# Optimization experiments

Measured on AMD Instinct MI355X. Metric: run time of the kernel, lower is better.

The kernel has to match this reference:

```python
import jax, jax.numpy as jnp
import numpy as np

D_MODEL = 1024
N_HEADS = 16
HEAD_DIM = D_MODEL // N_HEADS


def setup_inputs() -> dict:
    key = jax.random.key(0)
    k_x, k_qkv, k_out = jax.random.split(key, 3)
    B, T = 4, 2048
    x = jax.random.normal(k_x, (B, T, D_MODEL), dtype=jnp.float32)
    # nn.Linear weight is (out, in); we store transposed (in, out) for x @ W
    s = 1.0 / np.sqrt(D_MODEL)
    W_qkv = jax.random.uniform(k_qkv, (D_MODEL, 3 * D_MODEL), dtype=jnp.float32, minval=-s, maxval=s)
    W_out = jax.random.uniform(k_out, (D_MODEL, D_MODEL), dtype=jnp.float32, minval=-s, maxval=s)
    return {"x": x, "W_qkv": W_qkv, "W_out": W_out}


def reference(x, W_qkv, W_out):
    B, T, C = x.shape
    H, Dh = N_HEADS, HEAD_DIM
    qkv = x @ W_qkv                                   # (B,T,3C)
    q, k, v = jnp.split(qkv, 3, axis=-1)
    # (B,T,C) -> (B,H,T,Dh)
    def split_heads(t):
        return t.reshape(B, T, H, Dh).transpose(0, 2, 1, 3)
    q, k, v = split_heads(q), split_heads(k), split_heads(v)
    scale = 1.0 / np.sqrt(Dh).astype(np.float32)
    scores = jnp.einsum('bhqd,bhkd->bhqk', q, k) * scale  # (B,H,T,T)
    causal = jnp.triu(jnp.ones((T, T), dtype=bool), k=1)   # True above diag
    scores = jnp.where(causal, -jnp.inf, scores)
    attn = jax.nn.softmax(scores, axis=-1)
    out = jnp.einsum('bhqk,bhkd->bhqd', attn, v)       # (B,H,T,Dh)
    out = out.transpose(0, 2, 1, 3).reshape(B, T, C)
    return out @ W_out
```

## Files before the change

kernel.cpp:

```cpp
#include <hip/hip_runtime.h>
#include <stdint.h>

#define T_ 2048
#define BB_ 4

typedef __bf16 bf16x8 __attribute__((ext_vector_type(8)));
typedef float f32x4 __attribute__((ext_vector_type(4)));
typedef unsigned short u16x8 __attribute__((ext_vector_type(8)));
typedef unsigned int u32x2 __attribute__((ext_vector_type(2)));
typedef unsigned int u32x4 __attribute__((ext_vector_type(4)));

__device__ __forceinline__ unsigned short f2b(float f) {
    unsigned int u = __builtin_bit_cast(unsigned int, f);
    return (unsigned short)((u + 0x7fffu + ((u >> 16) & 1u)) >> 16);
}

__device__ __forceinline__ unsigned cvt_pk(float lo, float hi) {
    unsigned r;
    asm("v_cvt_pk_bf16_f32 %0, %1, %2" : "=v"(r) : "v"(lo), "v"(hi));
    return r;
}

__device__ __forceinline__ void gload16(const void* g, const void* lds) {
    __builtin_amdgcn_global_load_lds(
        (__attribute__((address_space(1))) void*)(uintptr_t)g,
        (__attribute__((address_space(3))) void*)(uintptr_t)(unsigned int)(uintptr_t)lds,
        16, 0, 0);
}

__device__ __forceinline__ bf16x8 ld_b8(const unsigned short* p) {
    return *(const bf16x8*)p;
}

#define MFMA16(a, b, c) __builtin_amdgcn_mfma_f32_16x16x32_bf16((a), (b), (c), 0, 0, 0)

__global__ __launch_bounds__(256) void k_cvt(const float* __restrict__ in,
                                             unsigned short* __restrict__ out, int n) {
    int i = (blockIdx.x * 256 + threadIdx.x) * 4;
    const int stride = gridDim.x * 256 * 4;
    for (; i < n; i += stride) {
        const float4 v = *(const float4*)(in + i);
        ushort4 o = make_ushort4(f2b(v.x), f2b(v.y), f2b(v.z), f2b(v.w));
        *(ushort4*)(out + i) = o;
    }
}

template <int K, int N>
__global__ __launch_bounds__(256) void k_cvt_T(const float* __restrict__ W,
                                               unsigned short* __restrict__ WT) {
    __shared__ unsigned short t_[64][72];
    const int nt = blockIdx.x % (N / 64), kt = blockIdx.x / (N / 64);
    const int tid = threadIdx.x;
    const int r = tid >> 2, c = (tid & 3) * 16;
    const float* src = W + (size_t)(kt * 64 + r) * N + nt * 64 + c;
#pragma unroll
    for (int j = 0; j < 16; j += 4) {
        float4 v = *(const float4*)(src + j);
        t_[r][c + j + 0] = f2b(v.x);
        t_[r][c + j + 1] = f2b(v.y);
        t_[r][c + j + 2] = f2b(v.z);
        t_[r][c + j + 3] = f2b(v.w);
    }
    __syncthreads();
    unsigned short* dst = WT + (size_t)(nt * 64 + r) * K + kt * 64 + c;
#pragma unroll
    for (int j = 0; j < 16; ++j) dst[j] = t_[c + j][r];
}

template <int MODE, int NCOLS>
__global__ __launch_bounds__(512, 2) void k_gemm256(
    const unsigned short* __restrict__ A, const unsigned short* __restrict__ Bt,
    void* __restrict__ Cv, unsigned short* __restrict__ vt2) {
    constexpr int K = 1024, NT = K / 64;
    __shared__ unsigned short Abuf[3][2][8192];
    __shared__ unsigned short Bbuf[3][8192];
    const int tid = threadIdx.x;
    const int lane = tid & 63, wid = tid >> 6;
    const int wr = wid >> 1, wc = wid & 1;
    const int l4 = lane >> 4, l15 = lane & 15;
    const int bid = blockIdx.y * gridDim.x + blockIdx.x;
    const int cpx = (gridDim.x * gridDim.y) >> 3;
    const int nb = (bid & 7) * cpx + (bid >> 3);
    const int m0 = (nb / gridDim.x) * 256, n0 = (nb % gridDim.x) * 128;

    const int se0 = tid * 8, se1 = tid * 8 + 4096;
    const int r0_ = se0 >> 6, c0_ = (se0 & 63) ^ ((r0_ & 7) << 3);
    const int r1_ = se1 >> 6, c1_ = (se1 & 63) ^ ((r1_ & 7) << 3);

    f32x4 acc[4][4] = {};

    auto STAGE1 = [&](int t, int d) {
        const unsigned short* as = A + (size_t)m0 * K + t * 64;
        gload16(as + (size_t)r0_ * K + c0_, &Abuf[d][0][se0]);
        gload16(as + (size_t)r1_ * K + c1_, &Abuf[d][0][se1]);
        const unsigned short* bs = Bt + (size_t)n0 * K + t * 64;
        gload16(bs + (size_t)r0_ * K + c0_, &Bbuf[d][se0]);
    };
    auto STAGE2 = [&](int t, int d) {
        const unsigned short* as = A + (size_t)(m0 + 128) * K + t * 64;
        gload16(as + (size_t)r0_ * K + c0_, &Abuf[d][1][se0]);
        gload16(as + (size_t)r1_ * K + c1_, &Abuf[d][1][se1]);
        const unsigned short* bs = Bt + (size_t)n0 * K + t * 64;
        gload16(bs + (size_t)r1_ * K + c1_, &Bbuf[d][se1]);
    };

    auto swz = [](const unsigned short* base, int row, int col) {
        int byte = row * 128 + col * 2;
        byte ^= (row & 7) << 4;
        return (const unsigned short*)((const char*)base + byte);
    };

    STAGE1(0, 0);
    STAGE2(0, 0);
    STAGE1(1, 1);
    STAGE2(1, 1);
    int d = 0;
    for (int t = 0; t < NT; ++t) {
        if (t == NT - 1)
            asm volatile("s_waitcnt vmcnt(0)" ::: "memory");
        else
            asm volatile("s_waitcnt vmcnt(6)" ::: "memory");
        __builtin_amdgcn_sched_barrier(0);
        __builtin_amdgcn_s_barrier();
        __builtin_amdgcn_sched_barrier(0);
        const int dn = (d + 2 >= 3) ? d - 1 : d + 2;
        if (t + 2 < NT) STAGE1(t + 2, dn);
        __builtin_amdgcn_sched_barrier(0);
        const unsigned short* Ah = &Abuf[d][wr >> 1][0];
        const unsigned short* Bh = &Bbuf[d][0];
        bf16x8 af[2][4], bfr[2][4];
#pragma unroll
        for (int ks = 0; ks < 2; ++ks) {
#pragma unroll
            for (int m = 0; m < 4; ++m)
                af[ks][m] =
                    ld_b8(swz(Ah, (wr & 1) * 64 + m * 16 + l15, ks * 32 + l4 * 8));
#pragma unroll
            for (int n = 0; n < 4; ++n)
                bfr[ks][n] = ld_b8(swz(Bh, wc * 64 + n * 16 + l15, ks * 32 + l4 * 8));
        }
        __builtin_amdgcn_s_setprio(1);
#pragma unroll
        for (int m = 0; m < 4; ++m)
#pragma unroll
            for (int n = 0; n < 4; ++n)
                acc[m][n] = MFMA16(af[0][m], bfr[0][n], acc[m][n]);
        __builtin_amdgcn_s_setprio(0);
        __builtin_amdgcn_sched_barrier(0);
        if (t + 2 < NT) STAGE2(t + 2, dn);
        __builtin_amdgcn_sched_barrier(0);
        __builtin_amdgcn_s_setprio(1);
#pragma unroll
        for (int m = 0; m < 4; ++m)
#pragma unroll
            for (int n = 0; n < 4; ++n)
                acc[m][n] = MFMA16(af[1][m], bfr[1][n], acc[m][n]);
        __builtin_amdgcn_s_setprio(0);
        d = (d + 1 == 3) ? 0 : d + 1;
    }

    const int crow0 = m0 + wr * 64 + l4 * 4;
    const int ccol0 = n0 + wc * 64 + l15;
    if (MODE == 0 && n0 >= 2048) {
#pragma unroll
        for (int m = 0; m < 4; ++m)
#pragma unroll
            for (int n = 0; n < 4; ++n) {
                const int row = crow0 + m * 16;
                const int c = ccol0 + n * 16 - 2048;
                const int b = row >> 11, tt = row & 2047;
                const int h = c >> 6, dh = c & 63;
                ushort4 o;
                o.x = f2b(acc[m][n][0]);
                o.y = f2b(acc[m][n][1]);
                o.z = f2b(acc[m][n][2]);
                o.w = f2b(acc[m][n][3]);
                *(ushort4*)(vt2 + (size_t)(b * 16 + h) * 131072 + (tt >> 2) * 256 +
                            dh * 4) = o;
            }
    } else {
#pragma unroll
        for (int m = 0; m < 4; ++m)
#pragma unroll
            for (int n = 0; n < 4; ++n)
#pragma unroll
                for (int r = 0; r < 4; ++r) {
                    const size_t idx =
                        (size_t)(crow0 + m * 16 + r) * NCOLS + ccol0 + n * 16;
                    if (MODE == 1)
                        ((float*)Cv)[idx] = acc[m][n][r];
                    else
                        ((unsigned short*)Cv)[idx] = f2b(acc[m][n][r]);
                }
    }
}

__global__ __launch_bounds__(512) void k_attn(const unsigned short* __restrict__ qkv,
                                              const unsigned short* __restrict__ vt2,
                                              unsigned short* __restrict__ ao) {
    __shared__ unsigned short Ks[2 * 4096];
    __shared__ unsigned short Vs[2 * 4096];
    const int bh = blockIdx.x & 63;
    const int p = blockIdx.x >> 6;
    const int b = bh >> 4, h = bh & 15;
    const int tid = threadIdx.x, lane = tid & 63, w = tid >> 6;
    const int l4 = lane >> 4, l15 = lane & 15;
    const int wrow = w * 16 + l15;

    const int sr0 = w * 8 + (lane >> 3);
    const int scol = 8 * ((lane & 7) ^ (lane >> 3));
    const unsigned short* Kg = qkv + (size_t)(b * T_) * 3072 + 1024 + h * 64;

    const unsigned short* Vg = vt2 + (size_t)bh * 131072;
    const int sv = w * 2 + (lane >> 5);
    const unsigned short* vsrcw =
        Vg + (4 * (sv & 3) + (sv >> 2)) * 256 + (lane & 31) * 8;

    const u32x4 onesw = {0x3f803f80u, 0x3f803f80u, 0x3f803f80u, 0x3f803f80u};
    const bf16x8 ones = __builtin_bit_cast(bf16x8, onesw);

    for (int half = 0; half < 2; ++half) {
        const int qq = half ? p : 15 - p;

        const unsigned short* qb =
            qkv + (size_t)(b * T_ + qq * 128 + wrow) * 3072 + h * 64;
        bf16x8 qf0, qf1;
        {
            const bf16x8 r0 = ld_b8(qb + l4 * 8);
            const bf16x8 r1 = ld_b8(qb + 32 + l4 * 8);
#pragma unroll
            for (int j = 0; j < 8; ++j) {
                qf0[j] = (__bf16)((float)r0[j] * 0.18033688f);
                qf1[j] = (__bf16)((float)r1[j] * 0.18033688f);
            }
        }

        f32x4 o[4] = {};
        f32x4 o_l = {};

        auto STAGE = [&](int kt, int bi) {
            gload16(Kg + (size_t)(kt * 64 + sr0) * 3072 + scol,
                    Ks + bi * 4096 + w * 512);
            gload16(vsrcw + (size_t)kt * 4096, Vs + bi * 4096 + w * 512);
        };

        auto COMPUTE = [&](int bi, int dk) {
            const unsigned short* Kb = Ks + bi * 4096;
            const unsigned short* Vb = Vs + bi * 4096;
            float tv[4][4];
            __builtin_amdgcn_s_setprio(1);
#pragma unroll
            for (int i = 0; i < 4; ++i) {
                const int key = i * 16 + l15;
                const int sw = (key & 7) << 4;
                const bf16x8 kf0 = ld_b8(Kb + (key * 128 + ((l4 * 16) ^ sw)) / 2);
                const bf16x8 kf1 = ld_b8(Kb + (key * 128 + ((l4 * 16 + 64) ^ sw)) / 2);
                f32x4 sacc = {};
                sacc = MFMA16(kf0, qf0, sacc);
                sacc = MFMA16(kf1, qf1, sacc);
#pragma unroll
                for (int r = 0; r < 4; ++r) tv[i][r] = sacc[r];
            }
            __builtin_amdgcn_s_setprio(0);
            if (dk >= 0) {
                const int base = dk * 64 - wrow;
#pragma unroll
                for (int i = 0; i < 4; ++i)
#pragma unroll
                    for (int r = 0; r < 4; ++r)
                        if (base + i * 16 + l4 * 4 + r > 0) tv[i][r] = -1e30f;
            }
            unsigned pw[8];
#pragma unroll
            for (int i = 0; i < 4; ++i) {
                float pv[4];
#pragma unroll
                for (int r = 0; r < 4; ++r) pv[r] = __builtin_amdgcn_exp2f(tv[i][r]);
                pw[i * 2 + 0] = cvt_pk(pv[0], pv[1]);
                pw[i * 2 + 1] = cvt_pk(pv[2], pv[3]);
            }
            __builtin_amdgcn_s_setprio(1);
#pragma unroll
            for (int st = 0; st < 2; ++st) {
                const u32x4 pk = {pw[st * 4 + 0], pw[st * 4 + 1], pw[st * 4 + 2],
                                  pw[st * 4 + 3]};
                const bf16x8 pf = __builtin_bit_cast(bf16x8, pk);
                o_l = MFMA16(pf, ones, o_l);
#pragma unroll
                for (int ni = 0; ni < 4; ++ni) {
                    const unsigned short* vb =
                        Vb + (l4 * 4 + st * 2) * 256 + (ni * 16 + l15) * 4;
                    const u32x2 va = *(const u32x2*)vb;
                    const u32x2 vc = *(const u32x2*)(vb + 256);
                    const u32x4 vv = {va.x, va.y, vc.x, vc.y};
                    const bf16x8 vf = __builtin_bit_cast(bf16x8, vv);
                    o[ni] = MFMA16(pf, vf, o[ni]);
                }
            }
            __builtin_amdgcn_s_setprio(0);
        };

        const int NTI = 2 * qq + 1;
        __syncthreads();
        STAGE(0, 0);
        __syncthreads();
        for (int kt = 0; kt < NTI; ++kt) {
            STAGE(kt + 1, (kt + 1) & 1);
            COMPUTE(kt & 1, kt - 2 * qq);
            __syncthreads();
        }
        COMPUTE(NTI & 1, 1);

        unsigned short* aop =
            ao + (size_t)(b * T_ + qq * 128 + w * 16) * 1024 + h * 64;
#pragma unroll
        for (int r = 0; r < 4; ++r) {
            const float inv = 1.0f / o_l[r];
#pragma unroll
            for (int ni = 0; ni < 4; ++ni)
                aop[(size_t)(l4 * 4 + r) * 1024 + ni * 16 + l15] = f2b(o[ni][r] * inv);
        }
    }
}

extern "C" void kernel_launch(void* const* d_in, const int* in_sizes, int n_in,
                              void* d_out, int out_size, void* d_ws, size_t ws_size,
                              hipStream_t stream) {
    (void)in_sizes; (void)n_in; (void)out_size; (void)ws_size;
    const float* x = (const float*)d_in[0];
    const float* Wqkv = (const float*)d_in[1];
    const float* Wout = (const float*)d_in[2];
    char* ws = (char*)d_ws;
    unsigned short* xb = (unsigned short*)(ws + 0);
    unsigned short* wqkvT = (unsigned short*)(ws + 16777216);
    unsigned short* woutT = (unsigned short*)(ws + 23068672);
    unsigned short* qkvb = (unsigned short*)(ws + 25165824);
    unsigned short* vt2 = (unsigned short*)(ws + 75497472);
    unsigned short* ao = (unsigned short*)(ws + 92274688);

    k_cvt<<<2048, 256, 0, stream>>>(x, xb, 4 * T_ * 1024);
    k_cvt_T<1024, 3072><<<16 * 48, 256, 0, stream>>>(Wqkv, wqkvT);
    k_cvt_T<1024, 1024><<<16 * 16, 256, 0, stream>>>(Wout, woutT);
    k_gemm256<0, 3072><<<dim3(24, 32), 512, 0, stream>>>(xb, wqkvT, qkvb, vt2);
    k_attn<<<512, 512, 0, stream>>>(qkvb, vt2, ao);
    k_gemm256<1, 1024><<<dim3(8, 32), 512, 0, stream>>>(ao, woutT, d_out, nullptr);
}
```

Before: 144.7 us.

## Process two adjacent query tiles per attention block sharing K/V tiles

```diff
diff --git a/kernel.cpp b/kernel.cpp
--- a/kernel.cpp
+++ b/kernel.cpp
@@ -78,10 +78,7 @@
     const int lane = tid & 63, wid = tid >> 6;
     const int wr = wid >> 1, wc = wid & 1;
     const int l4 = lane >> 4, l15 = lane & 15;
-    const int bid = blockIdx.y * gridDim.x + blockIdx.x;
-    const int cpx = (gridDim.x * gridDim.y) >> 3;
-    const int nb = (bid & 7) * cpx + (bid >> 3);
-    const int m0 = (nb / gridDim.x) * 256, n0 = (nb % gridDim.x) * 128;
+    const int m0 = blockIdx.y * 256, n0 = blockIdx.x * 128;
 
     const int se0 = tid * 8, se1 = tid * 8 + 4096;
     const int r0_ = se0 >> 6, c0_ = (se0 & 63) ^ ((r0_ & 7) << 3);
@@ -195,13 +192,13 @@
     }
 }
 
-__global__ __launch_bounds__(512) void k_attn(const unsigned short* __restrict__ qkv,
-                                              const unsigned short* __restrict__ vt2,
-                                              unsigned short* __restrict__ ao) {
+__global__ __launch_bounds__(512, 4) void k_attn(
+    const unsigned short* __restrict__ qkv, const unsigned short* __restrict__ vt2,
+    unsigned short* __restrict__ ao) {
     __shared__ unsigned short Ks[2 * 4096];
     __shared__ unsigned short Vs[2 * 4096];
     const int bh = blockIdx.x & 63;
-    const int p = blockIdx.x >> 6;
+    const int qq = 7 - (blockIdx.x >> 6);
     const int b = bh >> 4, h = bh & 15;
     const int tid = threadIdx.x, lane = tid & 63, w = tid >> 6;
     const int l4 = lane >> 4, l15 = lane & 15;
@@ -219,73 +216,99 @@
     const u32x4 onesw = {0x3f803f80u, 0x3f803f80u, 0x3f803f80u, 0x3f803f80u};
     const bf16x8 ones = __builtin_bit_cast(bf16x8, onesw);
 
-    for (int half = 0; half < 2; ++half) {
-        const int qq = half ? p : 15 - p;
-
+    bf16x8 qf[2][2];
+#pragma unroll
+    for (int qa = 0; qa < 2; ++qa) {
         const unsigned short* qb =
-            qkv + (size_t)(b * T_ + qq * 128 + wrow) * 3072 + h * 64;
-        bf16x8 qf0, qf1;
-        {
-            const bf16x8 r0 = ld_b8(qb + l4 * 8);
-            const bf16x8 r1 = ld_b8(qb + 32 + l4 * 8);
-#pragma unroll
-            for (int j = 0; j < 8; ++j) {
-                qf0[j] = (__bf16)((float)r0[j] * 0.18033688f);
-                qf1[j] = (__bf16)((float)r1[j] * 0.18033688f);
-            }
-        }
-
-        f32x4 o[4] = {};
-        f32x4 o_l = {};
-
-        auto STAGE = [&](int kt, int bi) {
-            gload16(Kg + (size_t)(kt * 64 + sr0) * 3072 + scol,
-                    Ks + bi * 4096 + w * 512);
-            gload16(vsrcw + (size_t)kt * 4096, Vs + bi * 4096 + w * 512);
-        };
-
-        auto COMPUTE = [&](int bi, int dk) {
-            const unsigned short* Kb = Ks + bi * 4096;
-            const unsigned short* Vb = Vs + bi * 4096;
-            float tv[4][4];
-            __builtin_amdgcn_s_setprio(1);
-#pragma unroll
-            for (int i = 0; i < 4; ++i) {
-                const int key = i * 16 + l15;
-                const int sw = (key & 7) << 4;
-                const bf16x8 kf0 = ld_b8(Kb + (key * 128 + ((l4 * 16) ^ sw)) / 2);
-                const bf16x8 kf1 = ld_b8(Kb + (key * 128 + ((l4 * 16 + 64) ^ sw)) / 2);
-                f32x4 sacc = {};
-                sacc = MFMA16(kf0, qf0, sacc);
-                sacc = MFMA16(kf1, qf1, sacc);
-#pragma unroll
-                for (int r = 0; r < 4; ++r) tv[i][r] = sacc[r];
-            }
-            __builtin_amdgcn_s_setprio(0);
-            if (dk >= 0) {
-                const int base = dk * 64 - wrow;
-#pragma unroll
-                for (int i = 0; i < 4; ++i)
-#pragma unroll
-                    for (int r = 0; r < 4; ++r)
-                        if (base + i * 16 + l4 * 4 + r > 0) tv[i][r] = -1e30f;
-            }
-            unsigned pw[8];
+            qkv + (size_t)(b * T_ + qq * 256 + qa * 128 + wrow) * 3072 + h * 64;
+        const bf16x8 r0 = ld_b8(qb + l4 * 8);
+        const bf16x8 r1 = ld_b8(qb + 32 + l4 * 8);
+#pragma unroll
+        for (int j = 0; j < 8; ++j) {
+            qf[qa][0][j] = (__bf16)((float)r0[j] * 0.18033688f);
+            qf[qa][1][j] = (__bf16)((float)r1[j] * 0.18033688f);
+        }
+    }
+
+    f32x4 o0[4] = {}, o1[4] = {};
+    f32x4 ol0 = {}, ol1 = {};
+
+    auto STAGE = [&](int kt, int bi) {
+        gload16(Kg + (size_t)(kt * 64 + sr0) * 3072 + scol, Ks + bi * 4096 + w * 512);
+        gload16(vsrcw + (size_t)kt * 4096, Vs + bi * 4096 + w * 512);
+    };
+
+    auto COMPUTE = [&](int bi, int dk) {
+        const unsigned short* Kb = Ks + bi * 4096;
+        const unsigned short* Vb = Vs + bi * 4096;
+        const bool do0 = dk < 2;
+        f32x4 tva[4], tvb[4];
+        __builtin_amdgcn_s_setprio(1);
+#pragma unroll
+        for (int i = 0; i < 4; ++i) {
+            const int key = i * 16 + l15;
+            const int sw = (key & 7) << 4;
+            const bf16x8 kf0 = ld_b8(Kb + (key * 128 + ((l4 * 16) ^ sw)) / 2);
+            const bf16x8 kf1 = ld_b8(Kb + (key * 128 + ((l4 * 16 + 64) ^ sw)) / 2);
+            f32x4 s1 = {};
+            s1 = MFMA16(kf0, qf[1][0], s1);
+            s1 = MFMA16(kf1, qf[1][1], s1);
+            tvb[i] = s1;
+            if (do0) {
+                f32x4 s0 = {};
+                s0 = MFMA16(kf0, qf[0][0], s0);
+                s0 = MFMA16(kf1, qf[0][1], s0);
+                tva[i] = s0;
+            }
+        }
+        __builtin_amdgcn_s_setprio(0);
+        if (do0 && dk >= 0) {
+            const int base = dk * 64 - wrow;
+#pragma unroll
+            for (int i = 0; i < 4; ++i)
+#pragma unroll
+                for (int r = 0; r < 4; ++r)
+                    if (base + i * 16 + l4 * 4 + r > 0) tva[i][r] = -1e30f;
+        }
+        if (dk >= 2) {
+            const int base = (dk - 2) * 64 - wrow;
+#pragma unroll
+            for (int i = 0; i < 4; ++i)
+#pragma unroll
+                for (int r = 0; r < 4; ++r)
+                    if (base + i * 16 + l4 * 4 + r > 0) tvb[i][r] = -1e30f;
+        }
+        unsigned pw0[8], pw1[8];
+#pragma unroll
+        for (int i = 0; i < 4; ++i) {
+            float pv[4];
+#pragma unroll
+            for (int r = 0; r < 4; ++r) pv[r] = __builtin_amdgcn_exp2f(tvb[i][r]);
+            pw1[i * 2 + 0] = cvt_pk(pv[0], pv[1]);
+            pw1[i * 2 + 1] = cvt_pk(pv[2], pv[3]);
+        }
+        if (do0) {
 #pragma unroll
             for (int i = 0; i < 4; ++i) {
                 float pv[4];
 #pragma unroll
-                for (int r = 0; r < 4; ++r) pv[r] = __builtin_amdgcn_exp2f(tv[i][r]);
-                pw[i * 2 + 0] = cvt_pk(pv[0], pv[1]);
-                pw[i * 2 + 1] = cvt_pk(pv[2], pv[3]);
-            }
-            __builtin_amdgcn_s_setprio(1);
-#pragma unroll
-            for (int st = 0; st < 2; ++st) {
-                const u32x4 pk = {pw[st * 4 + 0], pw[st * 4 + 1], pw[st * 4 + 2],
-                                  pw[st * 4 + 3]};
-                const bf16x8 pf = __builtin_bit_cast(bf16x8, pk);
-                o_l = MFMA16(pf, ones, o_l);
+                for (int r = 0; r < 4; ++r) pv[r] = __builtin_amdgcn_exp2f(tva[i][r]);
+                pw0[i * 2 + 0] = cvt_pk(pv[0], pv[1]);
+                pw0[i * 2 + 1] = cvt_pk(pv[2], pv[3]);
+            }
+        }
+        __builtin_amdgcn_s_setprio(1);
+#pragma unroll
+        for (int st = 0; st < 2; ++st) {
+            const u32x4 pk1 = {pw1[st * 4 + 0], pw1[st * 4 + 1], pw1[st * 4 + 2],
+                               pw1[st * 4 + 3]};
+            const bf16x8 pf1 = __builtin_bit_cast(bf16x8, pk1);
+            ol1 = MFMA16(pf1, ones, ol1);
+            if (do0) {
+                const u32x4 pk0 = {pw0[st * 4 + 0], pw0[st * 4 + 1], pw0[st * 4 + 2],
+                                   pw0[st * 4 + 3]};
+                const bf16x8 pf0 = __builtin_bit_cast(bf16x8, pk0);
+                ol0 = MFMA16(pf0, ones, ol0);
 #pragma unroll
                 for (int ni = 0; ni < 4; ++ni) {
                     const unsigned short* vb =
@@ -294,31 +317,47 @@
                     const u32x2 vc = *(const u32x2*)(vb + 256);
                     const u32x4 vv = {va.x, va.y, vc.x, vc.y};
                     const bf16x8 vf = __builtin_bit_cast(bf16x8, vv);
-                    o[ni] = MFMA16(pf, vf, o[ni]);
+                    o0[ni] = MFMA16(pf0, vf, o0[ni]);
+                    o1[ni] = MFMA16(pf1, vf, o1[ni]);
                 }
-            }
-            __builtin_amdgcn_s_setprio(0);
-        };
-
-        const int NTI = 2 * qq + 1;
+            } else {
+#pragma unroll
+                for (int ni = 0; ni < 4; ++ni) {
+                    const unsigned short* vb =
+                        Vb + (l4 * 4 + st * 2) * 256 + (ni * 16 + l15) * 4;
+                    const u32x2 va = *(const u32x2*)vb;
+                    const u32x2 vc = *(const u32x2*)(vb + 256);
+                    const u32x4 vv = {va.x, va.y, vc.x, vc.y};
+                    const bf16x8 vf = __builtin_bit_cast(bf16x8, vv);
+                    o1[ni] = MFMA16(pf1, vf, o1[ni]);
+                }
+            }
+        }
+        __builtin_amdgcn_s_setprio(0);
+    };
+
+    const int NTI = 4 * qq + 3;
+    STAGE(0, 0);
+    __syncthreads();
+    for (int kt = 0; kt < NTI; ++kt) {
+        STAGE(kt + 1, (kt + 1) & 1);
+        COMPUTE(kt & 1, kt - 4 * qq);
         __syncthreads();
-        STAGE(0, 0);
-        __syncthreads();
-        for (int kt = 0; kt < NTI; ++kt) {
-            STAGE(kt + 1, (kt + 1) & 1);
-            COMPUTE(kt & 1, kt - 2 * qq);
-            __syncthreads();
-        }
-        COMPUTE(NTI & 1, 1);
-
+    }
+    COMPUTE(NTI & 1, 3);
+
+#pragma unroll
+    for (int qa = 0; qa < 2; ++qa) {
         unsigned short* aop =
-            ao + (size_t)(b * T_ + qq * 128 + w * 16) * 1024 + h * 64;
+            ao + (size_t)(b * T_ + qq * 256 + qa * 128 + w * 16) * 1024 + h * 64;
 #pragma unroll
         for (int r = 0; r < 4; ++r) {
-            const float inv = 1.0f / o_l[r];
-#pragma unroll
-            for (int ni = 0; ni < 4; ++ni)
-                aop[(size_t)(l4 * 4 + r) * 1024 + ni * 16 + l15] = f2b(o[ni][r] * inv);
+            const float inv = 1.0f / (qa ? ol1[r] : ol0[r]);
+#pragma unroll
+            for (int ni = 0; ni < 4; ++ni) {
+                const float ov = qa ? o1[ni][r] : o0[ni][r];
+                aop[(size_t)(l4 * 4 + r) * 1024 + ni * 16 + l15] = f2b(ov * inv);
+            }
         }
     }
 }
```

New measurement: 148.6 us. 2.7% more time.

## Split GEMM K-step into four barrier-synchronized LDS-load/MFMA phases

Applied to the files above, without the earlier changes.

```diff
diff --git a/kernel.cpp b/kernel.cpp
--- a/kernel.cpp
+++ b/kernel.cpp
@@ -33,6 +33,7 @@
 }
 
 #define MFMA16(a, b, c) __builtin_amdgcn_mfma_f32_16x16x32_bf16((a), (b), (c), 0, 0, 0)
+#define SB() __builtin_amdgcn_sched_barrier(0)
 
 __global__ __launch_bounds__(256) void k_cvt(const float* __restrict__ in,
                                              unsigned short* __restrict__ out, int n) {
@@ -78,10 +79,7 @@
     const int lane = tid & 63, wid = tid >> 6;
     const int wr = wid >> 1, wc = wid & 1;
     const int l4 = lane >> 4, l15 = lane & 15;
-    const int bid = blockIdx.y * gridDim.x + blockIdx.x;
-    const int cpx = (gridDim.x * gridDim.y) >> 3;
-    const int nb = (bid & 7) * cpx + (bid >> 3);
-    const int m0 = (nb / gridDim.x) * 256, n0 = (nb % gridDim.x) * 128;
+    const int m0 = blockIdx.y * 256, n0 = blockIdx.x * 128;
 
     const int se0 = tid * 8, se1 = tid * 8 + 4096;
     const int r0_ = se0 >> 6, c0_ = (se0 & 63) ^ ((r0_ & 7) << 3);
@@ -120,42 +118,76 @@
             asm volatile("s_waitcnt vmcnt(0)" ::: "memory");
         else
             asm volatile("s_waitcnt vmcnt(6)" ::: "memory");
-        __builtin_amdgcn_sched_barrier(0);
-        __builtin_amdgcn_s_barrier();
-        __builtin_amdgcn_sched_barrier(0);
+        SB();
+        __builtin_amdgcn_s_barrier();
+        SB();
         const int dn = (d + 2 >= 3) ? d - 1 : d + 2;
-        if (t + 2 < NT) STAGE1(t + 2, dn);
-        __builtin_amdgcn_sched_barrier(0);
         const unsigned short* Ah = &Abuf[d][wr >> 1][0];
         const unsigned short* Bh = &Bbuf[d][0];
         bf16x8 af[2][4], bfr[2][4];
 #pragma unroll
-        for (int ks = 0; ks < 2; ++ks) {
-#pragma unroll
-            for (int m = 0; m < 4; ++m)
-                af[ks][m] =
-                    ld_b8(swz(Ah, (wr & 1) * 64 + m * 16 + l15, ks * 32 + l4 * 8));
-#pragma unroll
-            for (int n = 0; n < 4; ++n)
-                bfr[ks][n] = ld_b8(swz(Bh, wc * 64 + n * 16 + l15, ks * 32 + l4 * 8));
-        }
+        for (int m = 0; m < 4; ++m)
+            af[0][m] = ld_b8(swz(Ah, (wr & 1) * 64 + m * 16 + l15, l4 * 8));
+#pragma unroll
+        for (int n = 0; n < 2; ++n)
+            bfr[0][n] = ld_b8(swz(Bh, wc * 64 + n * 16 + l15, l4 * 8));
+        if (t + 2 < NT) STAGE1(t + 2, dn);
+        SB();
+        __builtin_amdgcn_s_barrier();
         __builtin_amdgcn_s_setprio(1);
 #pragma unroll
         for (int m = 0; m < 4; ++m)
 #pragma unroll
-            for (int n = 0; n < 4; ++n)
+            for (int n = 0; n < 2; ++n)
                 acc[m][n] = MFMA16(af[0][m], bfr[0][n], acc[m][n]);
         __builtin_amdgcn_s_setprio(0);
-        __builtin_amdgcn_sched_barrier(0);
+        SB();
+        __builtin_amdgcn_s_barrier();
+#pragma unroll
+        for (int n = 2; n < 4; ++n)
+            bfr[0][n] = ld_b8(swz(Bh, wc * 64 + n * 16 + l15, l4 * 8));
+        SB();
+        __builtin_amdgcn_s_barrier();
+        __builtin_amdgcn_s_setprio(1);
+#pragma unroll
+        for (int m = 0; m < 4; ++m)
+#pragma unroll
+            for (int n = 2; n < 4; ++n)
+                acc[m][n] = MFMA16(af[0][m], bfr[0][n], acc[m][n]);
+        __builtin_amdgcn_s_setprio(0);
+        SB();
+        __builtin_amdgcn_s_barrier();
+#pragma unroll
+        for (int m = 0; m < 4; ++m)
+            af[1][m] = ld_b8(swz(Ah, (wr & 1) * 64 + m * 16 + l15, 32 + l4 * 8));
+#pragma unroll
+        for (int n = 0; n < 2; ++n)
+            bfr[1][n] = ld_b8(swz(Bh, wc * 64 + n * 16 + l15, 32 + l4 * 8));
         if (t + 2 < NT) STAGE2(t + 2, dn);
-        __builtin_amdgcn_sched_barrier(0);
+        SB();
+        __builtin_amdgcn_s_barrier();
         __builtin_amdgcn_s_setprio(1);
 #pragma unroll
         for (int m = 0; m < 4; ++m)
 #pragma unroll
-            for (int n = 0; n < 4; ++n)
+            for (int n = 0; n < 2; ++n)
                 acc[m][n] = MFMA16(af[1][m], bfr[1][n], acc[m][n]);
         __builtin_amdgcn_s_setprio(0);
+        SB();
+        __builtin_amdgcn_s_barrier();
+#pragma unroll
+        for (int n = 2; n < 4; ++n)
+            bfr[1][n] = ld_b8(swz(Bh, wc * 64 + n * 16 + l15, 32 + l4 * 8));
+        SB();
+        __builtin_amdgcn_s_barrier();
+        __builtin_amdgcn_s_setprio(1);
+#pragma unroll
+        for (int m = 0; m < 4; ++m)
+#pragma unroll
+            for (int n = 2; n < 4; ++n)
+                acc[m][n] = MFMA16(af[1][m], bfr[1][n], acc[m][n]);
+        __builtin_amdgcn_s_setprio(0);
+        SB();
         d = (d + 1 == 3) ? 0 : d + 1;
     }
 
```

After: 149.2 us. 1.03x slower.
